# Performance work log

Measured on AMD Instinct MI355X. Metric: run time of the kernel, lower is better.

Reference implementation:

```python
import jax, jax.numpy as jnp
import numpy as np

B, IN, OUT, P = 512, 4096, 4096, 4
BITS = 4
MAX_INT = float(2 ** (BITS - 1) - 1)  # 7.0


def setup_inputs() -> dict:
    key = jax.random.key(0)
    k1, k2, k3, k4 = jax.random.split(key, 4)
    x = jax.random.normal(k1, (B, IN), dtype=jnp.float32)
    # Cached LFSR-generated pseudo-random matrix, values normalized to [-1, 1]
    U = jax.random.uniform(k2, (OUT * IN, P), dtype=jnp.float32, minval=-1.0, maxval=1.0)
    # 4-bit quantized projection: integers in [-7, 7] stored as float
    q = jnp.round(jnp.clip(jax.random.normal(k3, (P,), dtype=jnp.float32) * 3.0, -MAX_INT, MAX_INT))
    b = jax.random.normal(k4, (OUT,), dtype=jnp.float32)
    return {"x": x, "U": U, "q": q, "b": b, "exponent": 0}


def reference(x, U, q, b, exponent):
    # dequantize: t_hat = q / max_int * 2^exponent  (shared-exponent 4-bit dequant)
    scale = jnp.float32(2.0) ** exponent
    t_hat = q / MAX_INT * scale                      # [P]
    # reconstruct full weight: W = U @ t_hat, reshape to (out, in)
    w = (U @ t_hat).reshape(OUT, IN)                 # [OUT, IN]
    # original layer forward (nn.Linear): y = x @ W^T + b
    return x @ w.T + b                               # [B, OUT]
```

## Files before the change

kernel.cpp:

```cpp
#include <hip/hip_runtime.h>
#include <hip/hip_bf16.h>

typedef unsigned short ushort_t;
typedef unsigned int uint_t;
typedef __attribute__((ext_vector_type(4))) float f32x4;
typedef __attribute__((ext_vector_type(8))) short bf16x8;

#define B_DIM 512
#define IN_DIM 4096
#define OUT_DIM 4096
#define BN 32
#define BK 32
#define KSPLIT 8

__device__ __forceinline__ ushort_t f2bf(float f) {
    union { float f; uint_t u; } v; v.f = f;
    uint_t r = v.u + 0x7fffu + ((v.u >> 16) & 1u);
    return (ushort_t)(r >> 16);
}

__device__ __forceinline__ void async_copy16(void* lds, const void* g) {
    __builtin_amdgcn_global_load_lds(
        (const __attribute__((address_space(1))) uint_t*)g,
        (__attribute__((address_space(3))) uint_t*)lds, 16, 0, 0);
}

__global__ __launch_bounds__(256) void conv_x(const float4* __restrict__ X4,
                                              ushort_t* __restrict__ Xb) {
    size_t i = (size_t)blockIdx.x * 256 + threadIdx.x;
    float4 a = X4[i];
    ushort_t r[4] = { f2bf(a.x), f2bf(a.y), f2bf(a.z), f2bf(a.w) };
    *(uint2*)(Xb + i * 4) = *(const uint2*)r;
}

__global__ __launch_bounds__(256, 3) void gemm_fused(
    const ushort_t* __restrict__ A,
    const float4* __restrict__ U4,
    const float* __restrict__ q,
    const int* __restrict__ expo,
    float* __restrict__ part)
{
    const int M = B_DIM, N = OUT_DIM, K = IN_DIM;
    __shared__ ushort_t sA[B_DIM * BK];
    __shared__ ushort_t sW[BN * BK];

    const int tid  = threadIdx.x;
    const int lane = tid & 63;
    const int wave = tid >> 6;

    const int n0 = blockIdx.x * BN;
    const int kseg = K / KSPLIT;
    const size_t kbase = (size_t)blockIdx.y * kseg;

    const float scale = exp2f((float)expo[0]) * (1.0f / 7.0f);
    const float t0 = q[0] * scale, t1 = q[1] * scale,
                t2 = q[2] * scale, t3 = q[3] * scale;

    const ushort_t* gA = A + (size_t)(wave * 128 + (lane >> 2)) * K + kbase + (lane & 3) * 8;
    ushort_t* lA = sA + wave * 128 * BK + lane * 8;

    const float4* gU = U4 + (size_t)(n0 + (tid >> 3)) * K + kbase + (tid & 7) * 4;
    ushort_t* lW = sW + (tid >> 3) * BK + (tid & 7) * 4;

    const int quad = lane >> 4;
    const int r16  = lane & 15;
    const ushort_t* fa = sA + (wave * 128 + r16) * BK + quad * 8;
    const ushort_t* fb = sW + r16 * BK + quad * 8;

    f32x4 acc[8][2] = {};

    const int nsteps = kseg / BK;
    for (int s = 0; s < nsteps; ++s) {
#pragma unroll
        for (int c = 0; c < 8; ++c)
            async_copy16(lA + c * 16 * BK, gA + (size_t)c * 16 * K);
        float4 u0 = gU[0], u1 = gU[1], u2 = gU[2], u3 = gU[3];
        gA += BK; gU += BK;
        ushort_t wq[4];
        wq[0] = f2bf(u0.x * t0 + u0.y * t1 + u0.z * t2 + u0.w * t3);
        wq[1] = f2bf(u1.x * t0 + u1.y * t1 + u1.z * t2 + u1.w * t3);
        wq[2] = f2bf(u2.x * t0 + u2.y * t1 + u2.z * t2 + u2.w * t3);
        wq[3] = f2bf(u3.x * t0 + u3.y * t1 + u3.z * t2 + u3.w * t3);
        *(uint2*)lW = *(const uint2*)wq;
        __syncthreads();

        bf16x8 bv0 = *(const bf16x8*)(fb);
        bf16x8 bv1 = *(const bf16x8*)(fb + 16 * BK);
#pragma unroll
        for (int i = 0; i < 8; ++i) {
            bf16x8 av = *(const bf16x8*)(fa + i * 16 * BK);
            acc[i][0] = __builtin_amdgcn_mfma_f32_16x16x32_bf16(av, bv0, acc[i][0], 0, 0, 0);
            acc[i][1] = __builtin_amdgcn_mfma_f32_16x16x32_bf16(av, bv1, acc[i][1], 0, 0, 0);
        }
        __syncthreads();
    }

    float* outp = part + (size_t)blockIdx.y * M * N;
#pragma unroll
    for (int i = 0; i < 8; ++i) {
        const int mrow = wave * 128 + i * 16 + quad * 4;
#pragma unroll
        for (int j = 0; j < 2; ++j) {
            const int ncol = n0 + j * 16 + r16;
            float* o = outp + (size_t)mrow * N + ncol;
#pragma unroll
            for (int r = 0; r < 4; ++r)
                o[(size_t)r * N] = acc[i][j][r];
        }
    }
}

__global__ __launch_bounds__(256) void reduce_bias(const float4* __restrict__ part,
                                                   const float4* __restrict__ bias,
                                                   float4* __restrict__ out) {
    const int MN4 = (B_DIM * OUT_DIM) / 4;
    int i = blockIdx.x * 256 + threadIdx.x;
    float4 bb = bias[i & 1023];
    float sx = bb.x, sy = bb.y, sz = bb.z, sw = bb.w;
#pragma unroll
    for (int k = 0; k < KSPLIT; ++k) {
        float4 p = part[i + (size_t)k * MN4];
        sx += p.x; sy += p.y; sz += p.z; sw += p.w;
    }
    float4 o; o.x = sx; o.y = sy; o.z = sz; o.w = sw;
    out[i] = o;
}

extern "C" void kernel_launch(void* const* d_in, const int* in_sizes, int n_in,
                              void* d_out, int out_size, void* d_ws, size_t ws_size,
                              hipStream_t stream) {
    const float* x    = (const float*)d_in[0];
    const float* U    = (const float*)d_in[1];
    const float* q    = (const float*)d_in[2];
    const float* b    = (const float*)d_in[3];
    const int*   expo = (const int*)d_in[4];
    float* out = (float*)d_out;

    char* ws = (char*)d_ws;
    ushort_t* Xb  = (ushort_t*)ws;
    float*    prt = (float*)(ws + 4194304);

    conv_x<<<2048, 256, 0, stream>>>((const float4*)x, Xb);
    gemm_fused<<<dim3(128, KSPLIT), 256, 0, stream>>>(Xb, (const float4*)U, q, expo, prt);
    reduce_bias<<<2048, 256, 0, stream>>>((const float4*)prt, (const float4*)b,
                                          (float4*)out);
}
```

Measured before the change: 431.0 us.

## Load GEMM operands directly into registers and drop LDS staging and barriers

Replaces the LDS-staged GEMM with a kernel that has each wave read its A fragments and U rows straight from global memory into registers. Each wave dequantizes the W tile itself, and the next step's U values are prefetched into registers one iteration ahead. This removes the shared-memory buffers and the two __syncthreads per k-step. The cost is that every wave in a block now loads and dequantizes the same 32-column U tile, so U cache traffic and VALU work per block rise fourfold. Register pressure also grows, and the launch bound drops to 2 blocks per CU.

```diff
diff --git a/kernel.cpp b/kernel.cpp
--- a/kernel.cpp
+++ b/kernel.cpp
@@ -19,12 +19,6 @@
     return (ushort_t)(r >> 16);
 }
 
-__device__ __forceinline__ void async_copy16(void* lds, const void* g) {
-    __builtin_amdgcn_global_load_lds(
-        (const __attribute__((address_space(1))) uint_t*)g,
-        (__attribute__((address_space(3))) uint_t*)lds, 16, 0, 0);
-}
-
 __global__ __launch_bounds__(256) void conv_x(const float4* __restrict__ X4,
                                               ushort_t* __restrict__ Xb) {
     size_t i = (size_t)blockIdx.x * 256 + threadIdx.x;
@@ -33,7 +27,7 @@
     *(uint2*)(Xb + i * 4) = *(const uint2*)r;
 }
 
-__global__ __launch_bounds__(256, 3) void gemm_fused(
+__global__ __launch_bounds__(256, 2) void gemm_direct(
     const ushort_t* __restrict__ A,
     const float4* __restrict__ U4,
     const float* __restrict__ q,
@@ -41,9 +35,6 @@
     float* __restrict__ part)
 {
     const int M = B_DIM, N = OUT_DIM, K = IN_DIM;
-    __shared__ ushort_t sA[B_DIM * BK];
-    __shared__ ushort_t sW[BN * BK];
-
     const int tid  = threadIdx.x;
     const int lane = tid & 63;
     const int wave = tid >> 6;
@@ -56,43 +47,60 @@
     const float t0 = q[0] * scale, t1 = q[1] * scale,
                 t2 = q[2] * scale, t3 = q[3] * scale;
 
-    const ushort_t* gA = A + (size_t)(wave * 128 + (lane >> 2)) * K + kbase + (lane & 3) * 8;
-    ushort_t* lA = sA + wave * 128 * BK + lane * 8;
-
-    const float4* gU = U4 + (size_t)(n0 + (tid >> 3)) * K + kbase + (tid & 7) * 4;
-    ushort_t* lW = sW + (tid >> 3) * BK + (tid & 7) * 4;
-
     const int quad = lane >> 4;
     const int r16  = lane & 15;
-    const ushort_t* fa = sA + (wave * 128 + r16) * BK + quad * 8;
-    const ushort_t* fb = sW + r16 * BK + quad * 8;
+
+    const ushort_t* pa = A + (size_t)(wave * 128 + r16) * K + kbase + quad * 8;
+    const float4* pu0 = U4 + (size_t)(n0 + r16) * K + kbase + quad * 8;
+    const float4* pu1 = pu0 + (size_t)16 * K;
 
     f32x4 acc[8][2] = {};
+    const int nsteps = kseg / BK;
 
-    const int nsteps = kseg / BK;
+    float4 ua[8], ub[8];
+#pragma unroll
+    for (int c = 0; c < 8; ++c) ua[c] = pu0[c];
+#pragma unroll
+    for (int c = 0; c < 8; ++c) ub[c] = pu1[c];
+
+#pragma unroll 1
     for (int s = 0; s < nsteps; ++s) {
+        const size_t koff = (size_t)(s + 1 < nsteps ? s + 1 : s) * BK;
+        const ushort_t* pas = pa + (size_t)s * BK;
+
+        bf16x8 av[8];
+#pragma unroll
+        for (int i = 0; i < 8; ++i)
+            av[i] = *(const bf16x8*)(pas + (size_t)i * 16 * K);
+
+        float4 na[8];
+#pragma unroll
+        for (int c = 0; c < 8; ++c) na[c] = pu0[koff + c];
+
+        bf16x8 bv0;
 #pragma unroll
         for (int c = 0; c < 8; ++c)
-            async_copy16(lA + c * 16 * BK, gA + (size_t)c * 16 * K);
-        float4 u0 = gU[0], u1 = gU[1], u2 = gU[2], u3 = gU[3];
-        gA += BK; gU += BK;
-        ushort_t wq[4];
-        wq[0] = f2bf(u0.x * t0 + u0.y * t1 + u0.z * t2 + u0.w * t3);
-        wq[1] = f2bf(u1.x * t0 + u1.y * t1 + u1.z * t2 + u1.w * t3);
-        wq[2] = f2bf(u2.x * t0 + u2.y * t1 + u2.z * t2 + u2.w * t3);
-        wq[3] = f2bf(u3.x * t0 + u3.y * t1 + u3.z * t2 + u3.w * t3);
-        *(uint2*)lW = *(const uint2*)wq;
-        __syncthreads();
+            bv0[c] = (short)f2bf(ua[c].x * t0 + ua[c].y * t1 +
+                                 ua[c].z * t2 + ua[c].w * t3);
 
-        bf16x8 bv0 = *(const bf16x8*)(fb);
-        bf16x8 bv1 = *(const bf16x8*)(fb + 16 * BK);
+        float4 nb[8];
+#pragma unroll
+        for (int c = 0; c < 8; ++c) nb[c] = pu1[koff + c];
+
+        bf16x8 bv1;
+#pragma unroll
+        for (int c = 0; c < 8; ++c)
+            bv1[c] = (short)f2bf(ub[c].x * t0 + ub[c].y * t1 +
+                                 ub[c].z * t2 + ub[c].w * t3);
+
 #pragma unroll
         for (int i = 0; i < 8; ++i) {
-            bf16x8 av = *(const bf16x8*)(fa + i * 16 * BK);
-            acc[i][0] = __builtin_amdgcn_mfma_f32_16x16x32_bf16(av, bv0, acc[i][0], 0, 0, 0);
-            acc[i][1] = __builtin_amdgcn_mfma_f32_16x16x32_bf16(av, bv1, acc[i][1], 0, 0, 0);
+            acc[i][0] = __builtin_amdgcn_mfma_f32_16x16x32_bf16(av[i], bv0, acc[i][0], 0, 0, 0);
+            acc[i][1] = __builtin_amdgcn_mfma_f32_16x16x32_bf16(av[i], bv1, acc[i][1], 0, 0, 0);
         }
-        __syncthreads();
+
+#pragma unroll
+        for (int c = 0; c < 8; ++c) { ua[c] = na[c]; ub[c] = nb[c]; }
     }
 
     float* outp = part + (size_t)blockIdx.y * M * N;
@@ -141,7 +149,7 @@
     float*    prt = (float*)(ws + 4194304);
 
     conv_x<<<2048, 256, 0, stream>>>((const float4*)x, Xb);
-    gemm_fused<<<dim3(128, KSPLIT), 256, 0, stream>>>(Xb, (const float4*)U, q, expo, prt);
+    gemm_direct<<<dim3(128, KSPLIT), 256, 0, stream>>>(Xb, (const float4*)U, q, expo, prt);
     reduce_bias<<<2048, 256, 0, stream>>>((const float4*)prt, (const float4*)b,
                                           (float4*)out);
 }
```

After: 662.0 us. +53.6%, slower.
